# Kernel tuning notes

Hardware: AMD Instinct MI355X
Metric: run time of the kernel (lower is better)

Reference implementation:

```python
import jax, jax.numpy as jnp
import numpy as np

B, TE, H = 32, 8192, 128  # batch, encoder seq len, hidden

def setup_inputs() -> dict:
    key = jax.random.key(0)
    k1, k2, k3, k4, k5 = jax.random.split(key, 5)
    return {
        "encoder_out_seq": jax.random.normal(k1, (B, TE, H), dtype=jnp.float32),
        "decoder_out_seq": jax.random.normal(k2, (B, 1, H), dtype=jnp.float32),
        "W_a": jax.random.normal(k3, (H, H), dtype=jnp.float32) * 0.05,
        "U_a": jax.random.normal(k4, (H, H), dtype=jnp.float32) * 0.05,
        "V_a": jax.random.normal(k5, (H, 1), dtype=jnp.float32) * 0.05,
    }

def reference(encoder_out_seq, decoder_out_seq, W_a, U_a, V_a):
    # W_a . s : [B, TE, H]
    Ws = jnp.einsum('beh,hk->bek', encoder_out_seq, W_a)
    # U_a . h : [B, 1, H] (single decoder step, broadcasts over TE)
    Uh = jnp.einsum('bdh,hk->bdk', decoder_out_seq, U_a)
    # energy scores: tanh then project to scalar -> [B, TE]
    scores = jnp.einsum('bek,ko->be', jnp.tanh(Ws + Uh), V_a)
    e_i = jax.nn.softmax(scores, axis=-1)            # [B, TE]
    c_i = jnp.einsum('be,beh->bh', e_i, encoder_out_seq)  # context [B, H]
    return (e_i, c_i)
```

## Files before the change

kernel.cpp:

```cpp
#include <hip/hip_runtime.h>
#include <hip/hip_bf16.h>

#define B_  32
#define TE_ 8192
#define H_  128
#define M_  (B_ * TE_)

typedef __bf16 bf16x8 __attribute__((ext_vector_type(8)));
typedef float  f32x4  __attribute__((ext_vector_type(4)));

#define WS_UH    0
#define WS_WP    4096
#define WS_LACC  (4096 + 8192)
#define WS_CACC  (WS_LACC + 32)

__device__ __forceinline__ float tanh_fast(float x) {
  x = fminf(10.f, fmaxf(-10.f, x));
  float e = __expf(2.f * x);
  return (e - 1.f) * __builtin_amdgcn_rcpf(e + 1.f);
}

__global__ __launch_bounds__(256) void prep_kernel(
    const float* __restrict__ dec, const float* __restrict__ U,
    const float* __restrict__ W, float* __restrict__ ws) {
  int tid = blockIdx.x * 256 + threadIdx.x;
  int b = tid >> 7, k = tid & 127;
  const float* dp = dec + b * H_;
  float s = 0.f;
  #pragma unroll 8
  for (int h = 0; h < H_; ++h) s += dp[h] * U[h * H_ + k];
  ws[WS_UH + tid] = s;

  ws[WS_CACC + tid] = 0.f;
  if (tid < 32) ws[WS_LACC + tid] = 0.f;

  __bf16* Wp = (__bf16*)(ws + WS_WP);
  for (int i = tid; i < H_ * H_; i += 4096) {
    int j = i & 7;
    int lane = (i >> 3) & 63;
    int f = i >> 9;
    int sK = f & 3, nt = f >> 2;
    int kk = sK * 32 + ((lane >> 4) & 3) * 8 + j;
    int nn = nt * 16 + (lane & 15);
    Wp[i] = (__bf16)W[kk * H_ + nn];
  }
}

__global__ __launch_bounds__(256, 4) void fused_kernel(
    const float* __restrict__ enc, const float* __restrict__ ws_in,
    const float* __restrict__ V, float* __restrict__ wout,
    float* __restrict__ ws) {
  __shared__ uint4 ldsW[2048];
  __shared__ float ldsUV[256];
  __shared__ float lsum[4];

  int t = threadIdx.x;
  int blockRow = blockIdx.x << 8;
  int b = blockRow >> 13;

  const uint4* wsrc = (const uint4*)(ws_in + WS_WP);
  for (int i = t; i < 2048; i += 256) ldsW[i] = wsrc[i];
  if (t < 128) ldsUV[t] = ws_in[WS_UH + b * H_ + t];
  else ldsUV[t] = V[t - 128];
  __syncthreads();

  int wave = t >> 6, lane = t & 63;
  int l15 = lane & 15, quad = lane >> 4;

  float cacc[32];
  #pragma unroll
  for (int k = 0; k < 32; ++k) cacc[k] = 0.f;
  float Lpart = 0.f;

  const f32x4* rp0 = (const f32x4*)(enc + (size_t)(blockRow + (wave << 4) + l15) * H_) + quad * 2;
  const int stripStride = 4 * 16 * (H_ / 4);

  f32x4 buf[8];
  #pragma unroll
  for (int s = 0; s < 4; ++s) {
    buf[2 * s]     = __builtin_nontemporal_load(rp0 + s * 8);
    buf[2 * s + 1] = __builtin_nontemporal_load(rp0 + s * 8 + 1);
  }

  #pragma unroll
  for (int it = 0; it < 4; ++it) {
    bf16x8 af[4];
    #pragma unroll
    for (int s = 0; s < 4; ++s) {
      f32x4 lo = buf[2 * s], hi = buf[2 * s + 1];
      bf16x8 a;
      a[0] = (__bf16)lo[0]; a[1] = (__bf16)lo[1]; a[2] = (__bf16)lo[2]; a[3] = (__bf16)lo[3];
      a[4] = (__bf16)hi[0]; a[5] = (__bf16)hi[1]; a[6] = (__bf16)hi[2]; a[7] = (__bf16)hi[3];
      af[s] = a;
    }
    if (it < 3) {
      const f32x4* rp = rp0 + (it + 1) * stripStride;
      #pragma unroll
      for (int s = 0; s < 4; ++s) {
        buf[2 * s]     = __builtin_nontemporal_load(rp + s * 8);
        buf[2 * s + 1] = __builtin_nontemporal_load(rp + s * 8 + 1);
      }
    }

    float p = 0.f;
    #pragma unroll
    for (int nt = 0; nt < 8; ++nt) {
      f32x4 acc = {0.f, 0.f, 0.f, 0.f};
      #pragma unroll
      for (int s = 0; s < 4; ++s) {
        union { uint4 u; bf16x8 v; } bw;
        bw.u = ldsW[(nt * 4 + s) * 64 + lane];
        acc = __builtin_amdgcn_mfma_f32_16x16x32_bf16(bw.v, af[s], acc, 0, 0, 0);
      }
      float4 u4 = ((const float4*)ldsUV)[nt * 4 + quad];
      float4 v4 = ((const float4*)(ldsUV + 128))[nt * 4 + quad];
      p += tanh_fast(acc[0] + u4.x) * v4.x;
      p += tanh_fast(acc[1] + u4.y) * v4.y;
      p += tanh_fast(acc[2] + u4.z) * v4.z;
      p += tanh_fast(acc[3] + u4.w) * v4.w;
    }
    p += __shfl_xor(p, 16, 64);
    p += __shfl_xor(p, 32, 64);
    float w = __expf(p);

    int rowBase = blockRow + ((it * 4 + wave) << 4);
    if (quad == 0) wout[rowBase + l15] = w;
    Lpart += w;

    #pragma unroll
    for (int s = 0; s < 4; ++s)
      #pragma unroll
      for (int j = 0; j < 8; ++j)
        cacc[s * 8 + j] += w * (float)af[s][j];
  }

  #pragma unroll
  for (int m = 1; m < 16; m <<= 1) {
    #pragma unroll
    for (int k = 0; k < 32; ++k)
      cacc[k] += __shfl_xor(cacc[k], m, 64);
  }
  Lpart += __shfl_xor(Lpart, 1, 64);
  Lpart += __shfl_xor(Lpart, 2, 64);
  Lpart += __shfl_xor(Lpart, 4, 64);
  Lpart += __shfl_xor(Lpart, 8, 64);

  __syncthreads();
  float* pcbuf = (float*)ldsW;
  if (l15 == 0) {
    #pragma unroll
    for (int s = 0; s < 4; ++s)
      #pragma unroll
      for (int j = 0; j < 8; ++j)
        pcbuf[wave * H_ + s * 32 + quad * 8 + j] = cacc[s * 8 + j];
  }
  if (lane == 0) lsum[wave] = Lpart;
  __syncthreads();

  if (t < H_) {
    float s = pcbuf[0 * H_ + t] + pcbuf[1 * H_ + t] + pcbuf[2 * H_ + t] + pcbuf[3 * H_ + t];
    atomicAdd(&ws[WS_CACC + b * H_ + t], s);
  }
  if (t == 0)
    atomicAdd(&ws[WS_LACC + b], lsum[0] + lsum[1] + lsum[2] + lsum[3]);
}

__global__ __launch_bounds__(256) void finalize_kernel(
    float* __restrict__ e, float* __restrict__ c, const float* __restrict__ ws) {
  int t = threadIdx.x;
  if (blockIdx.x < 256) {
    int i4 = blockIdx.x * 256 + t;
    int b = i4 >> 11;
    float inv = 1.f / ws[WS_LACC + b];
    float4 v = ((float4*)e)[i4];
    v.x *= inv; v.y *= inv; v.z *= inv; v.w *= inv;
    ((float4*)e)[i4] = v;
  } else {
    #pragma unroll
    for (int k = 0; k < 16; ++k) {
      int i = k * 256 + t;
      int b = i >> 7;
      c[i] = ws[WS_CACC + i] / ws[WS_LACC + b];
    }
  }
}

extern "C" void kernel_launch(void* const* d_in, const int* in_sizes, int n_in,
                              void* d_out, int out_size, void* d_ws, size_t ws_size,
                              hipStream_t stream) {
  const float* enc = (const float*)d_in[0];
  const float* dec = (const float*)d_in[1];
  const float* Wa  = (const float*)d_in[2];
  const float* Ua  = (const float*)d_in[3];
  const float* Va  = (const float*)d_in[4];

  float* out   = (float*)d_out;
  float* e_out = out;
  float* c_out = out + B_ * TE_;
  float* ws    = (float*)d_ws;

  prep_kernel<<<16, 256, 0, stream>>>(dec, Ua, Wa, ws);
  fused_kernel<<<M_ / 256, 256, 0, stream>>>(enc, ws, Va, e_out, ws);
  finalize_kernel<<<257, 256, 0, stream>>>(e_out, c_out, ws);
}
```

Baseline: 210.7 us.

## Coalesce encoder loads via LDS staging and restructure prep kernel

The fused kernel now reads each 16-row strip with fully coalesced contiguous 16-byte loads per lane, converts to bf16, and stages through a padded per-wave LDS buffer to rebuild the MFMA fragment layout. The first strip's loads are issued before the W/U/V LDS setup to overlap latency. Separately, the prep kernel caches U_a in LDS and spreads the W repack across 32 blocks, and the fused kernel's occupancy hint drops from 4 to 3 blocks per SIMD to allow the extra LDS. The cost is an extra LDS write/read round trip per strip and lower occupancy.

```diff
diff --git a/kernel.cpp b/kernel.cpp
--- a/kernel.cpp
+++ b/kernel.cpp
@@ -7,6 +7,7 @@
 #define M_  (B_ * TE_)
 
 typedef __bf16 bf16x8 __attribute__((ext_vector_type(8)));
+typedef __bf16 bf16x4 __attribute__((ext_vector_type(4)));
 typedef float  f32x4  __attribute__((ext_vector_type(4)));
 
 #define WS_UH    0
@@ -14,6 +15,8 @@
 #define WS_LACC  (4096 + 8192)
 #define WS_CACC  (WS_LACC + 32)
 
+#define SROW 272
+
 __device__ __forceinline__ float tanh_fast(float x) {
   x = fminf(10.f, fmaxf(-10.f, x));
   float e = __expf(2.f * x);
@@ -23,40 +26,56 @@
 __global__ __launch_bounds__(256) void prep_kernel(
     const float* __restrict__ dec, const float* __restrict__ U,
     const float* __restrict__ W, float* __restrict__ ws) {
-  int tid = blockIdx.x * 256 + threadIdx.x;
-  int b = tid >> 7, k = tid & 127;
-  const float* dp = dec + b * H_;
-  float s = 0.f;
-  #pragma unroll 8
-  for (int h = 0; h < H_; ++h) s += dp[h] * U[h * H_ + k];
-  ws[WS_UH + tid] = s;
-
-  ws[WS_CACC + tid] = 0.f;
-  if (tid < 32) ws[WS_LACC + tid] = 0.f;
-
-  __bf16* Wp = (__bf16*)(ws + WS_WP);
-  for (int i = tid; i < H_ * H_; i += 4096) {
-    int j = i & 7;
-    int lane = (i >> 3) & 63;
-    int f = i >> 9;
-    int sK = f & 3, nt = f >> 2;
-    int kk = sK * 32 + ((lane >> 4) & 3) * 8 + j;
-    int nn = nt * 16 + (lane & 15);
-    Wp[i] = (__bf16)W[kk * H_ + nn];
-  }
-}
-
-__global__ __launch_bounds__(256, 4) void fused_kernel(
+  __shared__ float ldsU[H_ * H_];
+  __shared__ float ldsd[H_];
+  int b = blockIdx.x, t = threadIdx.x;
+
+  float4* l4 = (float4*)ldsU;
+  const float4* g4 = (const float4*)U;
+  #pragma unroll
+  for (int i = 0; i < 16; ++i) l4[t + 256 * i] = g4[t + 256 * i];
+  if (t < 32) ((float4*)ldsd)[t] = ((const float4*)(dec + b * H_))[t];
+  __syncthreads();
+
+  if (t < H_) {
+    float s = 0.f;
+    #pragma unroll
+    for (int h = 0; h < H_; ++h) s += ldsd[h] * ldsU[h * H_ + t];
+    ws[WS_UH + b * H_ + t] = s;
+    ws[WS_CACC + b * H_ + t] = 0.f;
+  }
+  if (t == 0) ws[WS_LACC + b] = 0.f;
+
+  if (t < 64) {
+    int nt = b >> 2, sK = b & 3;
+    int kk0 = sK * 32 + ((t >> 4) & 3) * 8;
+    int nn = nt * 16 + (t & 15);
+    __bf16* Wp = (__bf16*)(ws + WS_WP);
+    #pragma unroll
+    for (int j = 0; j < 8; ++j)
+      Wp[(b * 64 + t) * 8 + j] = (__bf16)W[(kk0 + j) * H_ + nn];
+  }
+}
+
+__global__ __launch_bounds__(256, 3) void fused_kernel(
     const float* __restrict__ enc, const float* __restrict__ ws_in,
     const float* __restrict__ V, float* __restrict__ wout,
     float* __restrict__ ws) {
   __shared__ uint4 ldsW[2048];
   __shared__ float ldsUV[256];
   __shared__ float lsum[4];
-
-  int t = threadIdx.x;
+  __shared__ __align__(16) unsigned char ldsS[4][16 * SROW];
+
+  int t = threadIdx.x, wave = t >> 6, lane = t & 63;
+  int l15 = lane & 15, quad = lane >> 4;
   int blockRow = blockIdx.x << 8;
   int b = blockRow >> 13;
+
+  const char* gbase = (const char*)enc + (size_t)(blockRow + (wave << 4)) * (H_ * 4);
+  f32x4 ld[8];
+  #pragma unroll
+  for (int i = 0; i < 8; ++i)
+    ld[i] = __builtin_nontemporal_load((const f32x4*)(gbase + i * 1024 + lane * 16));
 
   const uint4* wsrc = (const uint4*)(ws_in + WS_WP);
   for (int i = t; i < 2048; i += 256) ldsW[i] = wsrc[i];
@@ -64,43 +83,38 @@
   else ldsUV[t] = V[t - 128];
   __syncthreads();
 
-  int wave = t >> 6, lane = t & 63;
-  int l15 = lane & 15, quad = lane >> 4;
-
   float cacc[32];
   #pragma unroll
   for (int k = 0; k < 32; ++k) cacc[k] = 0.f;
   float Lpart = 0.f;
 
-  const f32x4* rp0 = (const f32x4*)(enc + (size_t)(blockRow + (wave << 4) + l15) * H_) + quad * 2;
-  const int stripStride = 4 * 16 * (H_ / 4);
-
-  f32x4 buf[8];
-  #pragma unroll
-  for (int s = 0; s < 4; ++s) {
-    buf[2 * s]     = __builtin_nontemporal_load(rp0 + s * 8);
-    buf[2 * s + 1] = __builtin_nontemporal_load(rp0 + s * 8 + 1);
-  }
+  unsigned char* sb = ldsS[wave];
+  int wrhi = lane >> 5, wc = lane & 31;
 
   #pragma unroll
   for (int it = 0; it < 4; ++it) {
+    uint2 hp[8];
+    #pragma unroll
+    for (int i = 0; i < 8; ++i) {
+      union { bf16x4 h; uint2 u; } cv;
+      cv.h[0] = (__bf16)ld[i][0]; cv.h[1] = (__bf16)ld[i][1];
+      cv.h[2] = (__bf16)ld[i][2]; cv.h[3] = (__bf16)ld[i][3];
+      hp[i] = cv.u;
+    }
+    if (it < 3) {
+      #pragma unroll
+      for (int i = 0; i < 8; ++i)
+        ld[i] = __builtin_nontemporal_load(
+            (const f32x4*)(gbase + (it + 1) * 32768 + i * 1024 + lane * 16));
+    }
+    #pragma unroll
+    for (int i = 0; i < 8; ++i)
+      *(uint2*)(sb + (2 * i + wrhi) * SROW + wc * 8) = hp[i];
+
     bf16x8 af[4];
     #pragma unroll
-    for (int s = 0; s < 4; ++s) {
-      f32x4 lo = buf[2 * s], hi = buf[2 * s + 1];
-      bf16x8 a;
-      a[0] = (__bf16)lo[0]; a[1] = (__bf16)lo[1]; a[2] = (__bf16)lo[2]; a[3] = (__bf16)lo[3];
-      a[4] = (__bf16)hi[0]; a[5] = (__bf16)hi[1]; a[6] = (__bf16)hi[2]; a[7] = (__bf16)hi[3];
-      af[s] = a;
-    }
-    if (it < 3) {
-      const f32x4* rp = rp0 + (it + 1) * stripStride;
-      #pragma unroll
-      for (int s = 0; s < 4; ++s) {
-        buf[2 * s]     = __builtin_nontemporal_load(rp + s * 8);
-        buf[2 * s + 1] = __builtin_nontemporal_load(rp + s * 8 + 1);
-      }
-    }
+    for (int s = 0; s < 4; ++s)
+      af[s] = *(const bf16x8*)(sb + l15 * SROW + s * 64 + quad * 16);
 
     float p = 0.f;
     #pragma unroll
@@ -199,7 +213,7 @@
   float* c_out = out + B_ * TE_;
   float* ws    = (float*)d_ws;
 
-  prep_kernel<<<16, 256, 0, stream>>>(dec, Ua, Wa, ws);
+  prep_kernel<<<B_, 256, 0, stream>>>(dec, Ua, Wa, ws);
   fused_kernel<<<M_ / 256, 256, 0, stream>>>(enc, ws, Va, e_out, ws);
   finalize_kernel<<<257, 256, 0, stream>>>(e_out, c_out, ws);
 }
```

Measured after the change: 204.9 us. 2.8% less time.
